# Kernel tuning notes

Measured on AMD Instinct MI355X. Metric: run time of the kernel, lower is better.

Reference implementation:

```python
import jax, jax.numpy as jnp
import numpy as np

N_NODES = 40000
N_EDGES = 640000
IN_CH = 128
OUT_CH = 128
NUM_RBF = 64


def setup_inputs() -> dict:
    key = jax.random.key(0)
    ks = jax.random.split(key, 8)
    x = jax.random.normal(ks[0], (N_NODES, IN_CH), dtype=jnp.float32)
    edge_index = jax.random.randint(ks[1], (2, N_EDGES), 0, N_NODES, dtype=jnp.int64)
    edge_rbf = jax.random.uniform(ks[2], (N_EDGES, NUM_RBF), dtype=jnp.float32)
    s1 = 1.0 / np.sqrt(NUM_RBF)
    s2 = 1.0 / np.sqrt(OUT_CH)
    sl = 1.0 / np.sqrt(IN_CH)
    W1 = jax.random.normal(ks[3], (NUM_RBF, OUT_CH), dtype=jnp.float32) * s1
    b1 = jnp.zeros((OUT_CH,), dtype=jnp.float32)
    W2 = jax.random.normal(ks[4], (OUT_CH, OUT_CH), dtype=jnp.float32) * s2
    b2 = jnp.zeros((OUT_CH,), dtype=jnp.float32)
    Wl = jax.random.normal(ks[5], (IN_CH, OUT_CH), dtype=jnp.float32) * sl
    bl = jnp.zeros((OUT_CH,), dtype=jnp.float32)
    return {"x": x, "edge_index": edge_index, "edge_rbf": edge_rbf,
            "W1": W1, "b1": b1, "W2": W2, "b2": b2, "Wl": Wl, "bl": bl}


def reference(x, edge_index, edge_rbf, W1, b1, W2, b2, Wl, bl):
    # filter_net: Linear -> ReLU -> Linear on edge RBF features  [E, OUT_CH]
    weight = jnp.maximum(edge_rbf @ W1 + b1, 0.0) @ W2 + b2
    # node linear projection  [N, OUT_CH]
    h = x @ Wl + bl
    row, col = edge_index[0], edge_index[1]
    # gather source node features, modulate by continuous filter
    msg = h[col] * weight  # [E, OUT_CH]
    # scatter-sum messages onto destination nodes
    out = jax.ops.segment_sum(msg, row, num_segments=x.shape[0])
    return out
```

## Files before the change

### kernel.cpp

```cpp
#include <hip/hip_runtime.h>


#define N_NODES 40000
#define N_EDGES 640000
#define IN_CH 128
#define OUT_CH 128
#define NUM_RBF 64

#define TILE_M 64
#define NTILES (N_EDGES / TILE_M)
#define RBF_STR 72
#define T_STR 136
#define HV_STR 136
#define W1_STR 72
#define W2_STR 136
#define NSCB ((N_NODES + 255) / 256)
#define EDGE_GRID 1024

typedef __attribute__((ext_vector_type(8))) short bf16x8;
typedef __attribute__((ext_vector_type(16))) float f32x16;

__device__ __forceinline__ unsigned short f2bf(float f) {
  unsigned u = __float_as_uint(f);
  return (unsigned short)((u + 0x7FFFu + ((u >> 16) & 1u)) >> 16);
}
__device__ __forceinline__ float bf2f(unsigned short s) {
  return __uint_as_float(((unsigned)s) << 16);
}

__global__ __launch_bounds__(256) void node_linear_mfma(
    const float* __restrict__ x, const float* __restrict__ Wl,
    const float* __restrict__ bl, unsigned short* __restrict__ hbf) {
  __shared__ __align__(16) char pool[IN_CH * W2_STR * 2];
  const int t = threadIdx.x;
  const int lane = t & 63;
  const int l31 = lane & 31;
  const int lhalf = lane >> 5;
  const int wv = t >> 6;

  {
    unsigned short* sWT = (unsigned short*)pool;
    const int k2 = t >> 1;
    const int d0 = (t & 1) * 64;
#pragma unroll
    for (int i = 0; i < 16; ++i) {
      float4 v = *(const float4*)(Wl + k2 * OUT_CH + d0 + 4 * i);
      sWT[(d0 + 4 * i + 0) * W2_STR + k2] = f2bf(v.x);
      sWT[(d0 + 4 * i + 1) * W2_STR + k2] = f2bf(v.y);
      sWT[(d0 + 4 * i + 2) * W2_STR + k2] = f2bf(v.z);
      sWT[(d0 + 4 * i + 3) * W2_STR + k2] = f2bf(v.w);
    }
  }
  __syncthreads();
  const int nbase = wv * 32 + l31;
  bf16x8 BW[8];
  {
    const unsigned short* sWT = (const unsigned short*)pool;
#pragma unroll
    for (int kk = 0; kk < 8; ++kk)
      BW[kk] = *(const bf16x8*)&sWT[nbase * W2_STR + kk * 16 + lhalf * 8];
  }
  const float blv = bl[nbase];
  __syncthreads();

  const int rbase = blockIdx.x * TILE_M;
  unsigned short* sX = (unsigned short*)pool;
  {
    const int m = t >> 2;
    const int c0 = (t & 3) * 32;
    const float* src = x + (size_t)(rbase + m) * IN_CH + c0;
#pragma unroll
    for (int i = 0; i < 8; ++i) {
      float4 v = *(const float4*)(src + 4 * i);
      ushort4 p;
      p.x = f2bf(v.x); p.y = f2bf(v.y); p.z = f2bf(v.z); p.w = f2bf(v.w);
      *(ushort4*)&sX[m * T_STR + c0 + 4 * i] = p;
    }
  }
  __syncthreads();
#pragma unroll
  for (int mt = 0; mt < 2; ++mt) {
    f32x16 acc = {0.f, 0.f, 0.f, 0.f, 0.f, 0.f, 0.f, 0.f,
                  0.f, 0.f, 0.f, 0.f, 0.f, 0.f, 0.f, 0.f};
#pragma unroll
    for (int kk = 0; kk < 8; ++kk) {
      bf16x8 A = *(const bf16x8*)&sX[(mt * 32 + l31) * T_STR + kk * 16 + lhalf * 8];
      acc = __builtin_amdgcn_mfma_f32_32x32x16_bf16(A, BW[kk], acc, 0, 0, 0);
    }
#pragma unroll
    for (int r = 0; r < 16; ++r) {
      const int rowm = mt * 32 + (r & 3) + 8 * (r >> 2) + 4 * lhalf;
      hbf[(size_t)(rbase + rowm) * OUT_CH + nbase] = f2bf(acc[r] + blv);
    }
  }
}

__global__ void hist_kernel(const int* __restrict__ rowI, int* __restrict__ count) {
  int e = blockIdx.x * 256 + threadIdx.x;
  if (e < N_EDGES) atomicAdd(&count[rowI[e]], 1);
}

__global__ __launch_bounds__(256) void scan1_kernel(const int* __restrict__ count,
                                                    int* __restrict__ tscan,
                                                    int* __restrict__ bsum) {
  __shared__ int s[256];
  const int t = threadIdx.x;
  const int i = blockIdx.x * 256 + t;
  const int v = (i < N_NODES) ? count[i] : 0;
  s[t] = v;
  __syncthreads();
  for (int off = 1; off < 256; off <<= 1) {
    int u = (t >= off) ? s[t - off] : 0;
    __syncthreads();
    s[t] += u;
    __syncthreads();
  }
  if (i < N_NODES) tscan[i] = s[t];
  if (t == 255) bsum[blockIdx.x] = s[255];
}

__global__ __launch_bounds__(256) void scan2_kernel(const int* __restrict__ bsum,
                                                    int* __restrict__ boff) {
  __shared__ int s[256];
  const int t = threadIdx.x;
  const int v = (t < NSCB) ? bsum[t] : 0;
  s[t] = v;
  __syncthreads();
  for (int off = 1; off < 256; off <<= 1) {
    int u = (t >= off) ? s[t - off] : 0;
    __syncthreads();
    s[t] += u;
    __syncthreads();
  }
  if (t < NSCB) boff[t] = s[t] - v;
}

__global__ __launch_bounds__(256) void scan3_kernel(
    const int* __restrict__ count, const int* __restrict__ tscan,
    const int* __restrict__ boff, int* __restrict__ cursor) {
  const int i = blockIdx.x * 256 + threadIdx.x;
  if (i < N_NODES) cursor[i] = boff[blockIdx.x] + tscan[i] - count[i];
}

__global__ void scatter_kernel(const int* __restrict__ rowI,
                               const int* __restrict__ colI,
                               int* __restrict__ cursor,
                               int* __restrict__ eperm, int* __restrict__ dsts,
                               int* __restrict__ cols) {
  int e = blockIdx.x * 256 + threadIdx.x;
  if (e < N_EDGES) {
    const int r = rowI[e];
    const int p = atomicAdd(&cursor[r], 1);
    eperm[p] = e;
    dsts[p] = r;
    cols[p] = colI[e];
  }
}

template <bool SORTED>
__global__ __launch_bounds__(256, 4) void edge_fused_kernel(
    const int* __restrict__ eperm, const float* __restrict__ rbf,
    const float* __restrict__ W1, const float* __restrict__ b1,
    const float* __restrict__ W2, const float* __restrict__ b2,
    const unsigned short* __restrict__ hbf, const int* __restrict__ dsts,
    const int* __restrict__ cols, float* __restrict__ outp) {
  __shared__ __align__(16) char pool[IN_CH * W2_STR * 2];

  unsigned short* sHv = (unsigned short*)pool;
  unsigned short* sT = (unsigned short*)pool;
  unsigned short* sRbf = (unsigned short*)(pool + TILE_M * HV_STR * 2);
  int* sAux = (int*)(pool + TILE_M * HV_STR * 2 + TILE_M * RBF_STR * 2);

  const int t = threadIdx.x;
  const int lane = t & 63;
  const int l31 = lane & 31;
  const int lhalf = lane >> 5;
  const int wv = t >> 6;
  const int nbase = wv * 32 + l31;

  {
    unsigned short* sW1T = (unsigned short*)pool;
    const int k = t >> 2;
    const int c0 = (t & 3) * 32;
#pragma unroll
    for (int i = 0; i < 8; ++i) {
      float4 v = *(const float4*)(W1 + k * OUT_CH + c0 + 4 * i);
      sW1T[(c0 + 4 * i + 0) * W1_STR + k] = f2bf(v.x);
      sW1T[(c0 + 4 * i + 1) * W1_STR + k] = f2bf(v.y);
      sW1T[(c0 + 4 * i + 2) * W1_STR + k] = f2bf(v.z);
      sW1T[(c0 + 4 * i + 3) * W1_STR + k] = f2bf(v.w);
    }
  }
  __syncthreads();
  bf16x8 B1[4];
  {
    const unsigned short* sW1T = (const unsigned short*)pool;
#pragma unroll
    for (int kk = 0; kk < 4; ++kk)
      B1[kk] = *(const bf16x8*)&sW1T[nbase * W1_STR + kk * 16 + lhalf * 8];
  }
  __syncthreads();
  {
    unsigned short* sW2T = (unsigned short*)pool;
    const int k2 = t >> 1;
    const int d0 = (t & 1) * 64;
#pragma unroll
    for (int i = 0; i < 16; ++i) {
      float4 v = *(const float4*)(W2 + k2 * OUT_CH + d0 + 4 * i);
      sW2T[(d0 + 4 * i + 0) * W2_STR + k2] = f2bf(v.x);
      sW2T[(d0 + 4 * i + 1) * W2_STR + k2] = f2bf(v.y);
      sW2T[(d0 + 4 * i + 2) * W2_STR + k2] = f2bf(v.z);
      sW2T[(d0 + 4 * i + 3) * W2_STR + k2] = f2bf(v.w);
    }
  }
  __syncthreads();
  bf16x8 B2[8];
  {
    const unsigned short* sW2T = (const unsigned short*)pool;
#pragma unroll
    for (int kk = 0; kk < 8; ++kk)
      B2[kk] = *(const bf16x8*)&sW2T[nbase * W2_STR + kk * 16 + lhalf * 8];
  }
  const float b1v = b1[nbase];
  const float b2v = b2[nbase];

  for (int tile = blockIdx.x; tile < NTILES; tile += gridDim.x) {
    const int ebase = tile * TILE_M;
    __syncthreads();

    {
      const int m = t >> 2;
      const int ep = SORTED ? eperm[ebase + m] : (ebase + m);
      const int kq = (t & 3) * 16;
      const float* src = rbf + (size_t)ep * NUM_RBF + kq;
#pragma unroll
      for (int i = 0; i < 4; ++i) {
        float4 v = *(const float4*)(src + 4 * i);
        ushort4 p;
        p.x = f2bf(v.x); p.y = f2bf(v.y); p.z = f2bf(v.z); p.w = f2bf(v.w);
        *(ushort4*)&sRbf[m * RBF_STR + kq + 4 * i] = p;
      }
#pragma unroll
      for (int i = 0; i < 4; ++i) {
        const int chunk = t + 256 * i;
        const int row = chunk >> 4;
        const int c8 = (chunk & 15) * 8;
        const int col = cols[ebase + row];
        *(uint4*)&sHv[row * HV_STR + c8] =
            *(const uint4*)(hbf + (size_t)col * OUT_CH + c8);
      }
      if (t < TILE_M) sAux[t] = dsts[ebase + t];
    }
    __syncthreads();

    float hv[2][16];
#pragma unroll
    for (int mt = 0; mt < 2; ++mt)
#pragma unroll
      for (int r = 0; r < 16; ++r) {
        const int rowm = mt * 32 + (r & 3) + 8 * (r >> 2) + 4 * lhalf;
        hv[mt][r] = bf2f(sHv[rowm * HV_STR + nbase]);
      }
    __syncthreads();

#pragma unroll
    for (int mt = 0; mt < 2; ++mt) {
      f32x16 acc = {0.f, 0.f, 0.f, 0.f, 0.f, 0.f, 0.f, 0.f,
                    0.f, 0.f, 0.f, 0.f, 0.f, 0.f, 0.f, 0.f};
#pragma unroll
      for (int kk = 0; kk < 4; ++kk) {
        bf16x8 A = *(const bf16x8*)&sRbf[(mt * 32 + l31) * RBF_STR + kk * 16 + lhalf * 8];
        acc = __builtin_amdgcn_mfma_f32_32x32x16_bf16(A, B1[kk], acc, 0, 0, 0);
      }
#pragma unroll
      for (int r = 0; r < 16; ++r) {
        const int rowm = (r & 3) + 8 * (r >> 2) + 4 * lhalf;
        float v = acc[r] + b1v;
        v = v > 0.f ? v : 0.f;
        sT[(mt * 32 + rowm) * T_STR + nbase] = f2bf(v);
      }
    }
    __syncthreads();

    float sum = 0.f;
    int curd = -1;
#pragma unroll
    for (int mt = 0; mt < 2; ++mt) {
      f32x16 acc = {0.f, 0.f, 0.f, 0.f, 0.f, 0.f, 0.f, 0.f,
                    0.f, 0.f, 0.f, 0.f, 0.f, 0.f, 0.f, 0.f};
#pragma unroll
      for (int kk = 0; kk < 8; ++kk) {
        bf16x8 A = *(const bf16x8*)&sT[(mt * 32 + l31) * T_STR + kk * 16 + lhalf * 8];
        acc = __builtin_amdgcn_mfma_f32_32x32x16_bf16(A, B2[kk], acc, 0, 0, 0);
      }
#pragma unroll
      for (int r = 0; r < 16; ++r) {
        const int rowm = mt * 32 + (r & 3) + 8 * (r >> 2) + 4 * lhalf;
        const float m = hv[mt][r] * (acc[r] + b2v);
        const int d = sAux[rowm];
        if (d != curd) {
          if (curd >= 0) atomicAdd(&outp[(size_t)curd * OUT_CH + nbase], sum);
          curd = d;
          sum = m;
        } else {
          sum += m;
        }
      }
    }
    atomicAdd(&outp[(size_t)curd * OUT_CH + nbase], sum);
  }
}

extern "C" void kernel_launch(void* const* d_in, const int* in_sizes, int n_in,
                              void* d_out, int out_size, void* d_ws, size_t ws_size,
                              hipStream_t stream) {
  const float* x    = (const float*)d_in[0];
  const int*   eidx = (const int*)d_in[1];
  const float* rbf  = (const float*)d_in[2];
  const float* W1   = (const float*)d_in[3];
  const float* b1   = (const float*)d_in[4];
  const float* W2   = (const float*)d_in[5];
  const float* b2   = (const float*)d_in[6];
  const float* Wl   = (const float*)d_in[7];
  const float* bl   = (const float*)d_in[8];
  float* out = (float*)d_out;

  char* ws = (char*)d_ws;
  const size_t HBF_B = (size_t)N_NODES * OUT_CH * 2;
  const size_t EP_B = (size_t)N_EDGES * 4;
  const size_t CNT_B = (size_t)N_NODES * 4;
  const size_t BS_B = 4 * 256;
  const size_t need = HBF_B + 3 * EP_B + 3 * CNT_B + 2 * BS_B + 64;

  size_t off = 0;
  unsigned short* hbf = (unsigned short*)(ws + off); off += HBF_B;
  int* eperm  = (int*)(ws + off); off += EP_B;
  int* dsts   = (int*)(ws + off); off += EP_B;
  int* cols   = (int*)(ws + off); off += EP_B;
  int* count  = (int*)(ws + off); off += CNT_B;
  int* cursor = (int*)(ws + off); off += CNT_B;
  int* tscan  = (int*)(ws + off); off += CNT_B;
  int* bsum   = (int*)(ws + off); off += BS_B;
  int* boff   = (int*)(ws + off); off += BS_B;

  const int* rowI = eidx;
  const int* colI = eidx + N_EDGES;

  hipMemsetAsync(out, 0, (size_t)N_NODES * OUT_CH * sizeof(float), stream);
  node_linear_mfma<<<N_NODES / TILE_M, 256, 0, stream>>>(x, Wl, bl, hbf);

  if (ws_size >= need) {
    hipMemsetAsync(count, 0, CNT_B, stream);
    hist_kernel<<<(N_EDGES + 255) / 256, 256, 0, stream>>>(rowI, count);
    scan1_kernel<<<NSCB, 256, 0, stream>>>(count, tscan, bsum);
    scan2_kernel<<<1, 256, 0, stream>>>(bsum, boff);
    scan3_kernel<<<NSCB, 256, 0, stream>>>(count, tscan, boff, cursor);
    scatter_kernel<<<(N_EDGES + 255) / 256, 256, 0, stream>>>(
        rowI, colI, cursor, eperm, dsts, cols);
    edge_fused_kernel<true><<<EDGE_GRID, 256, 0, stream>>>(
        eperm, rbf, W1, b1, W2, b2, hbf, dsts, cols, out);
  } else {
    edge_fused_kernel<false><<<EDGE_GRID, 256, 0, stream>>>(
        nullptr, rbf, W1, b1, W2, b2, hbf, rowI, colI, out);
  }
}
```

Baseline: 399.4 us.

## Fuse all stages into one cooperative mega-kernel with grid syncs

Result: slower. 1.430 ms (+258.1%).

```diff
diff --git a/kernel.cpp b/kernel.cpp
--- a/kernel.cpp
+++ b/kernel.cpp
@@ -1,4 +1,7 @@
 #include <hip/hip_runtime.h>
+#include <hip/hip_cooperative_groups.h>
+
+namespace cg = cooperative_groups;
 
 
 #define N_NODES 40000
@@ -9,6 +12,7 @@
 
 #define TILE_M 64
 #define NTILES (N_EDGES / TILE_M)
+#define NB_NODE (N_NODES / TILE_M)
 #define RBF_STR 72
 #define T_STR 136
 #define HV_STR 136
@@ -26,6 +30,296 @@
 }
 __device__ __forceinline__ float bf2f(unsigned short s) {
   return __uint_as_float(((unsigned)s) << 16);
+}
+
+__global__ __launch_bounds__(256, 4) void mega_kernel(
+    const float* __restrict__ x, const int* __restrict__ eidx,
+    const float* __restrict__ rbf, const float* __restrict__ W1,
+    const float* __restrict__ b1, const float* __restrict__ W2,
+    const float* __restrict__ b2, const float* __restrict__ Wl,
+    const float* __restrict__ bl, unsigned short* __restrict__ hbf,
+    int* __restrict__ eperm, int* __restrict__ dsts, int* __restrict__ cols,
+    int* __restrict__ count, int* __restrict__ cursor, int* __restrict__ tscan,
+    int* __restrict__ bsum, int* __restrict__ boff, float* __restrict__ outp) {
+  cg::grid_group grid = cg::this_grid();
+  __shared__ __align__(16) char pool[IN_CH * W2_STR * 2];
+
+  const int t = threadIdx.x;
+  const int bid = blockIdx.x;
+  const int gsz = gridDim.x;
+  const int gtid = bid * 256 + t;
+  const int gthreads = gsz * 256;
+  const int lane = t & 63;
+  const int l31 = lane & 31;
+  const int lhalf = lane >> 5;
+  const int wv = t >> 6;
+  const int nbase = wv * 32 + l31;
+
+  const int* rowI = eidx;
+  const int* colI = eidx + N_EDGES;
+
+  {
+    int4 z = {0, 0, 0, 0};
+    for (int i = gtid; i < N_NODES / 4; i += gthreads) ((int4*)count)[i] = z;
+  }
+  __threadfence();
+  grid.sync();
+
+  if (bid < NB_NODE) {
+    {
+      unsigned short* sWT = (unsigned short*)pool;
+      const int k2 = t >> 1;
+      const int d0 = (t & 1) * 64;
+#pragma unroll
+      for (int i = 0; i < 16; ++i) {
+        float4 v = *(const float4*)(Wl + k2 * OUT_CH + d0 + 4 * i);
+        sWT[(d0 + 4 * i + 0) * W2_STR + k2] = f2bf(v.x);
+        sWT[(d0 + 4 * i + 1) * W2_STR + k2] = f2bf(v.y);
+        sWT[(d0 + 4 * i + 2) * W2_STR + k2] = f2bf(v.z);
+        sWT[(d0 + 4 * i + 3) * W2_STR + k2] = f2bf(v.w);
+      }
+    }
+    __syncthreads();
+    bf16x8 BW[8];
+    {
+      const unsigned short* sWT = (const unsigned short*)pool;
+#pragma unroll
+      for (int kk = 0; kk < 8; ++kk)
+        BW[kk] = *(const bf16x8*)&sWT[nbase * W2_STR + kk * 16 + lhalf * 8];
+    }
+    const float blv = bl[nbase];
+    __syncthreads();
+
+    const int rbase = bid * TILE_M;
+    unsigned short* sX = (unsigned short*)pool;
+    {
+      const int m = t >> 2;
+      const int c0 = (t & 3) * 32;
+      const float* src = x + (size_t)(rbase + m) * IN_CH + c0;
+#pragma unroll
+      for (int i = 0; i < 8; ++i) {
+        float4 v = *(const float4*)(src + 4 * i);
+        ushort4 p;
+        p.x = f2bf(v.x); p.y = f2bf(v.y); p.z = f2bf(v.z); p.w = f2bf(v.w);
+        *(ushort4*)&sX[m * T_STR + c0 + 4 * i] = p;
+      }
+    }
+    __syncthreads();
+#pragma unroll
+    for (int mt = 0; mt < 2; ++mt) {
+      f32x16 acc = {0.f, 0.f, 0.f, 0.f, 0.f, 0.f, 0.f, 0.f,
+                    0.f, 0.f, 0.f, 0.f, 0.f, 0.f, 0.f, 0.f};
+#pragma unroll
+      for (int kk = 0; kk < 8; ++kk) {
+        bf16x8 A = *(const bf16x8*)&sX[(mt * 32 + l31) * T_STR + kk * 16 + lhalf * 8];
+        acc = __builtin_amdgcn_mfma_f32_32x32x16_bf16(A, BW[kk], acc, 0, 0, 0);
+      }
+#pragma unroll
+      for (int r = 0; r < 16; ++r) {
+        const int rowm = mt * 32 + (r & 3) + 8 * (r >> 2) + 4 * lhalf;
+        hbf[(size_t)(rbase + rowm) * OUT_CH + nbase] = f2bf(acc[r] + blv);
+      }
+    }
+  } else {
+    for (int e = (bid - NB_NODE) * 256 + t; e < N_EDGES;
+         e += (gsz - NB_NODE) * 256)
+      atomicAdd(&count[rowI[e]], 1);
+  }
+  {
+    float4 z = {0.f, 0.f, 0.f, 0.f};
+    for (int i = gtid; i < N_NODES * OUT_CH / 4; i += gthreads)
+      ((float4*)outp)[i] = z;
+  }
+  __threadfence();
+  grid.sync();
+
+  if (bid < NSCB) {
+    int* s = (int*)pool;
+    const int i = bid * 256 + t;
+    const int v = (i < N_NODES) ? count[i] : 0;
+    s[t] = v;
+    __syncthreads();
+    for (int off = 1; off < 256; off <<= 1) {
+      int u = (t >= off) ? s[t - off] : 0;
+      __syncthreads();
+      s[t] += u;
+      __syncthreads();
+    }
+    if (i < N_NODES) tscan[i] = s[t];
+    if (t == 255) bsum[bid] = s[255];
+  }
+  __threadfence();
+  grid.sync();
+
+  if (bid == 0) {
+    int* s = (int*)pool;
+    const int v = (t < NSCB) ? bsum[t] : 0;
+    s[t] = v;
+    __syncthreads();
+    for (int off = 1; off < 256; off <<= 1) {
+      int u = (t >= off) ? s[t - off] : 0;
+      __syncthreads();
+      s[t] += u;
+      __syncthreads();
+    }
+    if (t < NSCB) boff[t] = s[t] - v;
+  }
+  __threadfence();
+  grid.sync();
+
+  if (bid < NSCB) {
+    const int i = bid * 256 + t;
+    if (i < N_NODES) cursor[i] = boff[bid] + tscan[i] - count[i];
+  }
+  __threadfence();
+  grid.sync();
+
+  for (int e = gtid; e < N_EDGES; e += gthreads) {
+    const int r = rowI[e];
+    const int p = atomicAdd(&cursor[r], 1);
+    eperm[p] = e;
+    dsts[p] = r;
+    cols[p] = colI[e];
+  }
+  __threadfence();
+  grid.sync();
+
+  unsigned short* sHv = (unsigned short*)pool;
+  unsigned short* sT = (unsigned short*)pool;
+  unsigned short* sRbf = (unsigned short*)(pool + TILE_M * HV_STR * 2);
+  int* sAux = (int*)(pool + TILE_M * HV_STR * 2 + TILE_M * RBF_STR * 2);
+
+  {
+    unsigned short* sW1T = (unsigned short*)pool;
+    const int k = t >> 2;
+    const int c0 = (t & 3) * 32;
+#pragma unroll
+    for (int i = 0; i < 8; ++i) {
+      float4 v = *(const float4*)(W1 + k * OUT_CH + c0 + 4 * i);
+      sW1T[(c0 + 4 * i + 0) * W1_STR + k] = f2bf(v.x);
+      sW1T[(c0 + 4 * i + 1) * W1_STR + k] = f2bf(v.y);
+      sW1T[(c0 + 4 * i + 2) * W1_STR + k] = f2bf(v.z);
+      sW1T[(c0 + 4 * i + 3) * W1_STR + k] = f2bf(v.w);
+    }
+  }
+  __syncthreads();
+  bf16x8 B1[4];
+  {
+    const unsigned short* sW1T = (const unsigned short*)pool;
+#pragma unroll
+    for (int kk = 0; kk < 4; ++kk)
+      B1[kk] = *(const bf16x8*)&sW1T[nbase * W1_STR + kk * 16 + lhalf * 8];
+  }
+  __syncthreads();
+  {
+    unsigned short* sW2T = (unsigned short*)pool;
+    const int k2 = t >> 1;
+    const int d0 = (t & 1) * 64;
+#pragma unroll
+    for (int i = 0; i < 16; ++i) {
+      float4 v = *(const float4*)(W2 + k2 * OUT_CH + d0 + 4 * i);
+      sW2T[(d0 + 4 * i + 0) * W2_STR + k2] = f2bf(v.x);
+      sW2T[(d0 + 4 * i + 1) * W2_STR + k2] = f2bf(v.y);
+      sW2T[(d0 + 4 * i + 2) * W2_STR + k2] = f2bf(v.z);
+      sW2T[(d0 + 4 * i + 3) * W2_STR + k2] = f2bf(v.w);
+    }
+  }
+  __syncthreads();
+  bf16x8 B2[8];
+  {
+    const unsigned short* sW2T = (const unsigned short*)pool;
+#pragma unroll
+    for (int kk = 0; kk < 8; ++kk)
+      B2[kk] = *(const bf16x8*)&sW2T[nbase * W2_STR + kk * 16 + lhalf * 8];
+  }
+  const float b1v = b1[nbase];
+  const float b2v = b2[nbase];
+
+  for (int tile = bid; tile < NTILES; tile += gsz) {
+    const int ebase = tile * TILE_M;
+    __syncthreads();
+
+    {
+      const int m = t >> 2;
+      const int ep = eperm[ebase + m];
+      const int kq = (t & 3) * 16;
+      const float* src = rbf + (size_t)ep * NUM_RBF + kq;
+#pragma unroll
+      for (int i = 0; i < 4; ++i) {
+        float4 v = *(const float4*)(src + 4 * i);
+        ushort4 p;
+        p.x = f2bf(v.x); p.y = f2bf(v.y); p.z = f2bf(v.z); p.w = f2bf(v.w);
+        *(ushort4*)&sRbf[m * RBF_STR + kq + 4 * i] = p;
+      }
+#pragma unroll
+      for (int i = 0; i < 4; ++i) {
+        const int chunk = t + 256 * i;
+        const int row = chunk >> 4;
+        const int c8 = (chunk & 15) * 8;
+        const int col = cols[ebase + row];
+        *(uint4*)&sHv[row * HV_STR + c8] =
+            *(const uint4*)(hbf + (size_t)col * OUT_CH + c8);
+      }
+      if (t < TILE_M) sAux[t] = dsts[ebase + t];
+    }
+    __syncthreads();
+
+    float hv[2][16];
+#pragma unroll
+    for (int mt = 0; mt < 2; ++mt)
+#pragma unroll
+      for (int r = 0; r < 16; ++r) {
+        const int rowm = mt * 32 + (r & 3) + 8 * (r >> 2) + 4 * lhalf;
+        hv[mt][r] = bf2f(sHv[rowm * HV_STR + nbase]);
+      }
+    __syncthreads();
+
+#pragma unroll
+    for (int mt = 0; mt < 2; ++mt) {
+      f32x16 acc = {0.f, 0.f, 0.f, 0.f, 0.f, 0.f, 0.f, 0.f,
+                    0.f, 0.f, 0.f, 0.f, 0.f, 0.f, 0.f, 0.f};
+#pragma unroll
+      for (int kk = 0; kk < 4; ++kk) {
+        bf16x8 A = *(const bf16x8*)&sRbf[(mt * 32 + l31) * RBF_STR + kk * 16 + lhalf * 8];
+        acc = __builtin_amdgcn_mfma_f32_32x32x16_bf16(A, B1[kk], acc, 0, 0, 0);
+      }
+#pragma unroll
+      for (int r = 0; r < 16; ++r) {
+        const int rowm = (r & 3) + 8 * (r >> 2) + 4 * lhalf;
+        float v = acc[r] + b1v;
+        v = v > 0.f ? v : 0.f;
+        sT[(mt * 32 + rowm) * T_STR + nbase] = f2bf(v);
+      }
+    }
+    __syncthreads();
+
+    float sum = 0.f;
+    int curd = -1;
+#pragma unroll
+    for (int mt = 0; mt < 2; ++mt) {
+      f32x16 acc = {0.f, 0.f, 0.f, 0.f, 0.f, 0.f, 0.f, 0.f,
+                    0.f, 0.f, 0.f, 0.f, 0.f, 0.f, 0.f, 0.f};
+#pragma unroll
+      for (int kk = 0; kk < 8; ++kk) {
+        bf16x8 A = *(const bf16x8*)&sT[(mt * 32 + l31) * T_STR + kk * 16 + lhalf * 8];
+        acc = __builtin_amdgcn_mfma_f32_32x32x16_bf16(A, B2[kk], acc, 0, 0, 0);
+      }
+#pragma unroll
+      for (int r = 0; r < 16; ++r) {
+        const int rowm = mt * 32 + (r & 3) + 8 * (r >> 2) + 4 * lhalf;
+        const float m = hv[mt][r] * (acc[r] + b2v);
+        const int d = sAux[rowm];
+        if (d != curd) {
+          if (curd >= 0) atomicAdd(&outp[(size_t)curd * OUT_CH + nbase], sum);
+          curd = d;
+          sum = m;
+        } else {
+          sum += m;
+        }
+      }
+    }
+    atomicAdd(&outp[(size_t)curd * OUT_CH + nbase], sum);
+  }
 }
 
 __global__ __launch_bounds__(256) void node_linear_mfma(
@@ -297,7 +591,7 @@
       for (int r = 0; r < 16; ++r) {
         const int rowm = mt * 32 + (r & 3) + 8 * (r >> 2) + 4 * lhalf;
         const float m = hv[mt][r] * (acc[r] + b2v);
-        const int d = sAux[rowm];
+        const int d = SORTED ? sAux[rowm] : dsts[ebase + rowm];
         if (d != curd) {
           if (curd >= 0) atomicAdd(&outp[(size_t)curd * OUT_CH + nbase], sum);
           curd = d;
@@ -346,10 +640,19 @@
   const int* rowI = eidx;
   const int* colI = eidx + N_EDGES;
 
-  hipMemsetAsync(out, 0, (size_t)N_NODES * OUT_CH * sizeof(float), stream);
-  node_linear_mfma<<<N_NODES / TILE_M, 256, 0, stream>>>(x, Wl, bl, hbf);
-
   if (ws_size >= need) {
+    void* kargs[] = {(void*)&x,     (void*)&eidx, (void*)&rbf,   (void*)&W1,
+                     (void*)&b1,    (void*)&W2,   (void*)&b2,    (void*)&Wl,
+                     (void*)&bl,    (void*)&hbf,  (void*)&eperm, (void*)&dsts,
+                     (void*)&cols,  (void*)&count, (void*)&cursor,
+                     (void*)&tscan, (void*)&bsum, (void*)&boff,  (void*)&out};
+    hipError_t err = hipLaunchCooperativeKernel(
+        mega_kernel, dim3(EDGE_GRID), dim3(256), kargs, 0, stream);
+    if (err == hipSuccess) return;
+    (void)hipGetLastError();
+
+    hipMemsetAsync(out, 0, (size_t)N_NODES * OUT_CH * sizeof(float), stream);
+    node_linear_mfma<<<NB_NODE, 256, 0, stream>>>(x, Wl, bl, hbf);
     hipMemsetAsync(count, 0, CNT_B, stream);
     hist_kernel<<<(N_EDGES + 255) / 256, 256, 0, stream>>>(rowI, count);
     scan1_kernel<<<NSCB, 256, 0, stream>>>(count, tscan, bsum);
@@ -360,6 +663,8 @@
     edge_fused_kernel<true><<<EDGE_GRID, 256, 0, stream>>>(
         eperm, rbf, W1, b1, W2, b2, hbf, dsts, cols, out);
   } else {
+    hipMemsetAsync(out, 0, (size_t)N_NODES * OUT_CH * sizeof(float), stream);
+    node_linear_mfma<<<NB_NODE, 256, 0, stream>>>(x, Wl, bl, hbf);
     edge_fused_kernel<false><<<EDGE_GRID, 256, 0, stream>>>(
         nullptr, rbf, W1, b1, W2, b2, hbf, rowI, colI, out);
   }
```

## Fuse launches, decoupled-lookback scan, packed edge keys, register prefetch

Applied to the files above, without the earlier changes.

Measured after the change: 496.6 us. 1.24x slower.

```diff
diff --git a/kernel.cpp b/kernel.cpp
--- a/kernel.cpp
+++ b/kernel.cpp
@@ -9,6 +9,7 @@
 
 #define TILE_M 64
 #define NTILES (N_EDGES / TILE_M)
+#define NB_NODE (N_NODES / TILE_M)
 #define RBF_STR 72
 #define T_STR 136
 #define HV_STR 136
@@ -16,6 +17,8 @@
 #define W2_STR 136
 #define NSCB ((N_NODES + 255) / 256)
 #define EDGE_GRID 1024
+#define K1_GRID 1024
+#define ZC_BLOCKS 32
 
 typedef __attribute__((ext_vector_type(8))) short bf16x8;
 typedef __attribute__((ext_vector_type(16))) float f32x16;
@@ -28,15 +31,39 @@
   return __uint_as_float(((unsigned)s) << 16);
 }
 
-__global__ __launch_bounds__(256) void node_linear_mfma(
+__global__ __launch_bounds__(256) void k1_kernel(
     const float* __restrict__ x, const float* __restrict__ Wl,
-    const float* __restrict__ bl, unsigned short* __restrict__ hbf) {
+    const float* __restrict__ bl, unsigned short* __restrict__ hbf,
+    int* __restrict__ count, float* __restrict__ outp) {
   __shared__ __align__(16) char pool[IN_CH * W2_STR * 2];
+  const int bid = blockIdx.x;
   const int t = threadIdx.x;
+
+  if (bid >= NB_NODE) {
+    if (bid < NB_NODE + ZC_BLOCKS) {
+      if (count) {
+        int4 z = {0, 0, 0, 0};
+        for (int i = (bid - NB_NODE) * 256 + t; i < N_NODES / 4;
+             i += ZC_BLOCKS * 256)
+          ((int4*)count)[i] = z;
+      }
+    } else {
+      if (outp) {
+        float4 z = {0.f, 0.f, 0.f, 0.f};
+        const int nb = K1_GRID - NB_NODE - ZC_BLOCKS;
+        for (int i = (bid - NB_NODE - ZC_BLOCKS) * 256 + t;
+             i < N_NODES * OUT_CH / 4; i += nb * 256)
+          ((float4*)outp)[i] = z;
+      }
+    }
+    return;
+  }
+
   const int lane = t & 63;
   const int l31 = lane & 31;
   const int lhalf = lane >> 5;
   const int wv = t >> 6;
+  const int nbase = wv * 32 + l31;
 
   {
     unsigned short* sWT = (unsigned short*)pool;
@@ -52,7 +79,6 @@
     }
   }
   __syncthreads();
-  const int nbase = wv * 32 + l31;
   bf16x8 BW[8];
   {
     const unsigned short* sWT = (const unsigned short*)pool;
@@ -63,7 +89,7 @@
   const float blv = bl[nbase];
   __syncthreads();
 
-  const int rbase = blockIdx.x * TILE_M;
+  const int rbase = bid * TILE_M;
   unsigned short* sX = (unsigned short*)pool;
   {
     const int m = t >> 2;
@@ -95,17 +121,21 @@
   }
 }
 
-__global__ void hist_kernel(const int* __restrict__ rowI, int* __restrict__ count) {
+__global__ void hist_kernel(const int* __restrict__ rowI, int* __restrict__ count,
+                            unsigned long long* __restrict__ status) {
+  if (blockIdx.x == 0 && threadIdx.x < NSCB) status[threadIdx.x] = 0ULL;
   int e = blockIdx.x * 256 + threadIdx.x;
   if (e < N_EDGES) atomicAdd(&count[rowI[e]], 1);
 }
 
-__global__ __launch_bounds__(256) void scan1_kernel(const int* __restrict__ count,
-                                                    int* __restrict__ tscan,
-                                                    int* __restrict__ bsum) {
+__global__ __launch_bounds__(256) void scan_kernel(
+    const int* __restrict__ count, unsigned long long* __restrict__ status,
+    int* __restrict__ cursor) {
   __shared__ int s[256];
+  __shared__ int wsum[4];
   const int t = threadIdx.x;
-  const int i = blockIdx.x * 256 + t;
+  const int b = blockIdx.x;
+  const int i = b * 256 + t;
   const int v = (i < N_NODES) ? count[i] : 0;
   s[t] = v;
   __syncthreads();
@@ -115,55 +145,44 @@
     s[t] += u;
     __syncthreads();
   }
-  if (i < N_NODES) tscan[i] = s[t];
-  if (t == 255) bsum[blockIdx.x] = s[255];
-}
-
-__global__ __launch_bounds__(256) void scan2_kernel(const int* __restrict__ bsum,
-                                                    int* __restrict__ boff) {
-  __shared__ int s[256];
-  const int t = threadIdx.x;
-  const int v = (t < NSCB) ? bsum[t] : 0;
-  s[t] = v;
-  __syncthreads();
-  for (int off = 1; off < 256; off <<= 1) {
-    int u = (t >= off) ? s[t - off] : 0;
-    __syncthreads();
-    s[t] += u;
-    __syncthreads();
-  }
-  if (t < NSCB) boff[t] = s[t] - v;
-}
-
-__global__ __launch_bounds__(256) void scan3_kernel(
-    const int* __restrict__ count, const int* __restrict__ tscan,
-    const int* __restrict__ boff, int* __restrict__ cursor) {
-  const int i = blockIdx.x * 256 + threadIdx.x;
-  if (i < N_NODES) cursor[i] = boff[blockIdx.x] + tscan[i] - count[i];
+  if (t == 255)
+    __hip_atomic_store(&status[b], (1ULL << 32) | (unsigned)s[255],
+                       __ATOMIC_RELEASE, __HIP_MEMORY_SCOPE_AGENT);
+  int contrib = 0;
+  if (t < b) {
+    unsigned long long sv;
+    do {
+      sv = __hip_atomic_load(&status[t], __ATOMIC_ACQUIRE,
+                             __HIP_MEMORY_SCOPE_AGENT);
+    } while (!(sv >> 32));
+    contrib = (int)(unsigned)sv;
+  }
+  for (int o = 32; o > 0; o >>= 1) contrib += __shfl_down(contrib, o, 64);
+  if ((t & 63) == 0) wsum[t >> 6] = contrib;
+  __syncthreads();
+  const int boffv = wsum[0] + wsum[1] + wsum[2] + wsum[3];
+  if (i < N_NODES) cursor[i] = boffv + s[t] - v;
 }
 
 __global__ void scatter_kernel(const int* __restrict__ rowI,
                                const int* __restrict__ colI,
                                int* __restrict__ cursor,
-                               int* __restrict__ eperm, int* __restrict__ dsts,
-                               int* __restrict__ cols) {
+                               unsigned long long* __restrict__ packed) {
   int e = blockIdx.x * 256 + threadIdx.x;
   if (e < N_EDGES) {
     const int r = rowI[e];
+    const int c = colI[e];
     const int p = atomicAdd(&cursor[r], 1);
-    eperm[p] = e;
-    dsts[p] = r;
-    cols[p] = colI[e];
-  }
-}
-
-template <bool SORTED>
+    packed[p] = ((unsigned long long)r << 36) | ((unsigned long long)c << 20) |
+                (unsigned)e;
+  }
+}
+
 __global__ __launch_bounds__(256, 4) void edge_fused_kernel(
-    const int* __restrict__ eperm, const float* __restrict__ rbf,
+    const unsigned long long* __restrict__ packed, const float* __restrict__ rbf,
     const float* __restrict__ W1, const float* __restrict__ b1,
     const float* __restrict__ W2, const float* __restrict__ b2,
-    const unsigned short* __restrict__ hbf, const int* __restrict__ dsts,
-    const int* __restrict__ cols, float* __restrict__ outp) {
+    const unsigned short* __restrict__ hbf, float* __restrict__ outp) {
   __shared__ __align__(16) char pool[IN_CH * W2_STR * 2];
 
   unsigned short* sHv = (unsigned short*)pool;
@@ -224,15 +243,190 @@
   const float b1v = b1[nbase];
   const float b2v = b2[nbase];
 
+  const int m4 = t >> 2;
+  const int kq = (t & 3) * 16;
+
+  float4 rbfreg[4];
+  uint4 hvreg[4];
+  int auxv = 0;
+
+  auto prefetch = [&](int tl) {
+    const int eb = tl * TILE_M;
+    const unsigned long long pkm = packed[eb + m4];
+    const float* src = rbf + (size_t)(pkm & 0xFFFFFu) * NUM_RBF + kq;
+#pragma unroll
+    for (int i = 0; i < 4; ++i) rbfreg[i] = *(const float4*)(src + 4 * i);
+#pragma unroll
+    for (int i = 0; i < 4; ++i) {
+      const int chunk = t + 256 * i;
+      const int row = chunk >> 4;
+      const int c8 = (chunk & 15) * 8;
+      const unsigned long long pkr = packed[eb + row];
+      const int col = (int)((pkr >> 20) & 0xFFFFu);
+      hvreg[i] = *(const uint4*)(hbf + (size_t)col * OUT_CH + c8);
+    }
+    if (t < TILE_M) auxv = (int)(packed[eb + t] >> 36);
+  };
+
+  int tile = blockIdx.x;
+  if (tile < NTILES) prefetch(tile);
+
+  for (; tile < NTILES; tile += gridDim.x) {
+    __syncthreads();
+
+#pragma unroll
+    for (int i = 0; i < 4; ++i) {
+      float4 v = rbfreg[i];
+      ushort4 p;
+      p.x = f2bf(v.x); p.y = f2bf(v.y); p.z = f2bf(v.z); p.w = f2bf(v.w);
+      *(ushort4*)&sRbf[m4 * RBF_STR + kq + 4 * i] = p;
+    }
+#pragma unroll
+    for (int i = 0; i < 4; ++i) {
+      const int chunk = t + 256 * i;
+      const int row = chunk >> 4;
+      const int c8 = (chunk & 15) * 8;
+      *(uint4*)&sHv[row * HV_STR + c8] = hvreg[i];
+    }
+    if (t < TILE_M) sAux[t] = auxv;
+    __syncthreads();
+
+    const int tn = tile + gridDim.x;
+    if (tn < NTILES) prefetch(tn);
+
+    float hv[2][16];
+#pragma unroll
+    for (int mt = 0; mt < 2; ++mt)
+#pragma unroll
+      for (int r = 0; r < 16; ++r) {
+        const int rowm = mt * 32 + (r & 3) + 8 * (r >> 2) + 4 * lhalf;
+        hv[mt][r] = bf2f(sHv[rowm * HV_STR + nbase]);
+      }
+    __syncthreads();
+
+#pragma unroll
+    for (int mt = 0; mt < 2; ++mt) {
+      f32x16 acc = {0.f, 0.f, 0.f, 0.f, 0.f, 0.f, 0.f, 0.f,
+                    0.f, 0.f, 0.f, 0.f, 0.f, 0.f, 0.f, 0.f};
+#pragma unroll
+      for (int kk = 0; kk < 4; ++kk) {
+        bf16x8 A = *(const bf16x8*)&sRbf[(mt * 32 + l31) * RBF_STR + kk * 16 + lhalf * 8];
+        acc = __builtin_amdgcn_mfma_f32_32x32x16_bf16(A, B1[kk], acc, 0, 0, 0);
+      }
+#pragma unroll
+      for (int r = 0; r < 16; ++r) {
+        const int rowm = (r & 3) + 8 * (r >> 2) + 4 * lhalf;
+        float v = acc[r] + b1v;
+        v = v > 0.f ? v : 0.f;
+        sT[(mt * 32 + rowm) * T_STR + nbase] = f2bf(v);
+      }
+    }
+    __syncthreads();
+
+    float sum = 0.f;
+    int curd = -1;
+#pragma unroll
+    for (int mt = 0; mt < 2; ++mt) {
+      f32x16 acc = {0.f, 0.f, 0.f, 0.f, 0.f, 0.f, 0.f, 0.f,
+                    0.f, 0.f, 0.f, 0.f, 0.f, 0.f, 0.f, 0.f};
+#pragma unroll
+      for (int kk = 0; kk < 8; ++kk) {
+        bf16x8 A = *(const bf16x8*)&sT[(mt * 32 + l31) * T_STR + kk * 16 + lhalf * 8];
+        acc = __builtin_amdgcn_mfma_f32_32x32x16_bf16(A, B2[kk], acc, 0, 0, 0);
+      }
+#pragma unroll
+      for (int r = 0; r < 16; ++r) {
+        const int rowm = mt * 32 + (r & 3) + 8 * (r >> 2) + 4 * lhalf;
+        const float m = hv[mt][r] * (acc[r] + b2v);
+        const int d = sAux[rowm];
+        if (d != curd) {
+          if (curd >= 0) atomicAdd(&outp[(size_t)curd * OUT_CH + nbase], sum);
+          curd = d;
+          sum = m;
+        } else {
+          sum += m;
+        }
+      }
+    }
+    atomicAdd(&outp[(size_t)curd * OUT_CH + nbase], sum);
+  }
+}
+
+__global__ __launch_bounds__(256, 4) void edge_atomic_kernel(
+    const int* __restrict__ eidx, const float* __restrict__ rbf,
+    const float* __restrict__ W1, const float* __restrict__ b1,
+    const float* __restrict__ W2, const float* __restrict__ b2,
+    const unsigned short* __restrict__ hbf, float* __restrict__ outp) {
+  __shared__ __align__(16) char pool[IN_CH * W2_STR * 2];
+
+  unsigned short* sHv = (unsigned short*)pool;
+  unsigned short* sT = (unsigned short*)pool;
+  unsigned short* sRbf = (unsigned short*)(pool + TILE_M * HV_STR * 2);
+  int* sAux = (int*)(pool + TILE_M * HV_STR * 2 + TILE_M * RBF_STR * 2);
+
+  const int t = threadIdx.x;
+  const int lane = t & 63;
+  const int l31 = lane & 31;
+  const int lhalf = lane >> 5;
+  const int wv = t >> 6;
+  const int nbase = wv * 32 + l31;
+
+  {
+    unsigned short* sW1T = (unsigned short*)pool;
+    const int k = t >> 2;
+    const int c0 = (t & 3) * 32;
+#pragma unroll
+    for (int i = 0; i < 8; ++i) {
+      float4 v = *(const float4*)(W1 + k * OUT_CH + c0 + 4 * i);
+      sW1T[(c0 + 4 * i + 0) * W1_STR + k] = f2bf(v.x);
+      sW1T[(c0 + 4 * i + 1) * W1_STR + k] = f2bf(v.y);
+      sW1T[(c0 + 4 * i + 2) * W1_STR + k] = f2bf(v.z);
+      sW1T[(c0 + 4 * i + 3) * W1_STR + k] = f2bf(v.w);
+    }
+  }
+  __syncthreads();
+  bf16x8 B1[4];
+  {
+    const unsigned short* sW1T = (const unsigned short*)pool;
+#pragma unroll
+    for (int kk = 0; kk < 4; ++kk)
+      B1[kk] = *(const bf16x8*)&sW1T[nbase * W1_STR + kk * 16 + lhalf * 8];
+  }
+  __syncthreads();
+  {
+    unsigned short* sW2T = (unsigned short*)pool;
+    const int k2 = t >> 1;
+    const int d0 = (t & 1) * 64;
+#pragma unroll
+    for (int i = 0; i < 16; ++i) {
+      float4 v = *(const float4*)(W2 + k2 * OUT_CH + d0 + 4 * i);
+      sW2T[(d0 + 4 * i + 0) * W2_STR + k2] = f2bf(v.x);
+      sW2T[(d0 + 4 * i + 1) * W2_STR + k2] = f2bf(v.y);
+      sW2T[(d0 + 4 * i + 2) * W2_STR + k2] = f2bf(v.z);
+      sW2T[(d0 + 4 * i + 3) * W2_STR + k2] = f2bf(v.w);
+    }
+  }
+  __syncthreads();
+  bf16x8 B2[8];
+  {
+    const unsigned short* sW2T = (const unsigned short*)pool;
+#pragma unroll
+    for (int kk = 0; kk < 8; ++kk)
+      B2[kk] = *(const bf16x8*)&sW2T[nbase * W2_STR + kk * 16 + lhalf * 8];
+  }
+  const float b1v = b1[nbase];
+  const float b2v = b2[nbase];
+
+  const int* rowI = eidx;
+  const int* colI = eidx + N_EDGES;
+
   for (int tile = blockIdx.x; tile < NTILES; tile += gridDim.x) {
     const int ebase = tile * TILE_M;
     __syncthreads();
-
     {
       const int m = t >> 2;
-      const int ep = SORTED ? eperm[ebase + m] : (ebase + m);
       const int kq = (t & 3) * 16;
-      const float* src = rbf + (size_t)ep * NUM_RBF + kq;
+      const float* src = rbf + (size_t)(ebase + m) * NUM_RBF + kq;
 #pragma unroll
       for (int i = 0; i < 4; ++i) {
         float4 v = *(const float4*)(src + 4 * i);
@@ -245,11 +439,11 @@
         const int chunk = t + 256 * i;
         const int row = chunk >> 4;
         const int c8 = (chunk & 15) * 8;
-        const int col = cols[ebase + row];
+        const int col = colI[ebase + row];
         *(uint4*)&sHv[row * HV_STR + c8] =
             *(const uint4*)(hbf + (size_t)col * OUT_CH + c8);
       }
-      if (t < TILE_M) sAux[t] = dsts[ebase + t];
+      if (t < TILE_M) sAux[t] = rowI[ebase + t];
     }
     __syncthreads();
 
@@ -327,40 +521,33 @@
 
   char* ws = (char*)d_ws;
   const size_t HBF_B = (size_t)N_NODES * OUT_CH * 2;
-  const size_t EP_B = (size_t)N_EDGES * 4;
+  const size_t PK_B = (size_t)N_EDGES * 8;
   const size_t CNT_B = (size_t)N_NODES * 4;
-  const size_t BS_B = 4 * 256;
-  const size_t need = HBF_B + 3 * EP_B + 3 * CNT_B + 2 * BS_B + 64;
+  const size_t ST_B = 1280;
+  const size_t need = HBF_B + PK_B + 2 * CNT_B + ST_B + 64;
 
   size_t off = 0;
   unsigned short* hbf = (unsigned short*)(ws + off); off += HBF_B;
-  int* eperm  = (int*)(ws + off); off += EP_B;
-  int* dsts   = (int*)(ws + off); off += EP_B;
-  int* cols   = (int*)(ws + off); off += EP_B;
+  unsigned long long* packed = (unsigned long long*)(ws + off); off += PK_B;
   int* count  = (int*)(ws + off); off += CNT_B;
   int* cursor = (int*)(ws + off); off += CNT_B;
-  int* tscan  = (int*)(ws + off); off += CNT_B;
-  int* bsum   = (int*)(ws + off); off += BS_B;
-  int* boff   = (int*)(ws + off); off += BS_B;
+  unsigned long long* status = (unsigned long long*)(ws + off); off += ST_B;
 
   const int* rowI = eidx;
   const int* colI = eidx + N_EDGES;
 
-  hipMemsetAsync(out, 0, (size_t)N_NODES * OUT_CH * sizeof(float), stream);
-  node_linear_mfma<<<N_NODES / TILE_M, 256, 0, stream>>>(x, Wl, bl, hbf);
-
   if (ws_size >= need) {
-    hipMemsetAsync(count, 0, CNT_B, stream);
-    hist_kernel<<<(N_EDGES + 255) / 256, 256, 0, stream>>>(rowI, count);
-    scan1_kernel<<<NSCB, 256, 0, stream>>>(count, tscan, bsum);
-    scan2_kernel<<<1, 256, 0, stream>>>(bsum, boff);
-    scan3_kernel<<<NSCB, 256, 0, stream>>>(count, tscan, boff, cursor);
+    k1_kernel<<<K1_GRID, 256, 0, stream>>>(x, Wl, bl, hbf, count, out);
+    hist_kernel<<<(N_EDGES + 255) / 256, 256, 0, stream>>>(rowI, count, status);
+    scan_kernel<<<NSCB, 256, 0, stream>>>(count, status, cursor);
     scatter_kernel<<<(N_EDGES + 255) / 256, 256, 0, stream>>>(
-        rowI, colI, cursor, eperm, dsts, cols);
-    edge_fused_kernel<true><<<EDGE_GRID, 256, 0, stream>>>(
-        eperm, rbf, W1, b1, W2, b2, hbf, dsts, cols, out);
+        rowI, colI, cursor, packed);
+    edge_fused_kernel<<<EDGE_GRID, 256, 0, stream>>>(
+        packed, rbf, W1, b1, W2, b2, hbf, out);
   } else {
-    edge_fused_kernel<false><<<EDGE_GRID, 256, 0, stream>>>(
-        nullptr, rbf, W1, b1, W2, b2, hbf, rowI, colI, out);
-  }
-}
+    hipMemsetAsync(out, 0, (size_t)N_NODES * OUT_CH * sizeof(float), stream);
+    k1_kernel<<<NB_NODE, 256, 0, stream>>>(x, Wl, bl, hbf, nullptr, nullptr);
+    edge_atomic_kernel<<<EDGE_GRID, 256, 0, stream>>>(
+        eidx, rbf, W1, b1, W2, b2, hbf, out);
+  }
+}
```
